# Kernel optimization log

Measured on AMD Instinct MI355X. Metric: run time of the kernel, lower is better.

The kernel has to match this reference:

```python
import jax, jax.numpy as jnp
import numpy as np

# --- static config ---
B = 64        # graphs per batch
NPG = 512     # nodes per graph
N = B * NPG   # total nodes = 32768
EPG = 8192    # edges per graph (avg degree 16)
E = B * EPG   # total edges = 524288
L = 16        # tokens per node
V = 50000     # vocab
H = 256       # hidden_size == rnn hidden_size
P = 128       # projection_dim
K1 = 256      # ceil(0.5 * 512) nodes kept after pool 1
K2 = 128      # ceil(0.5 * 256) nodes kept after pool 2
PAD = 0


def setup_inputs() -> dict:
    key = jax.random.key(0)
    ks = jax.random.split(key, 16)
    tokens = jax.random.randint(ks[0], (N, L), 0, V, dtype=jnp.int32)
    eg = jnp.repeat(jnp.arange(B, dtype=jnp.int32), EPG)  # graph id per edge
    src = jax.random.randint(ks[1], (E,), 0, NPG, dtype=jnp.int32) + eg * NPG
    dst = jax.random.randint(ks[2], (E,), 0, NPG, dtype=jnp.int32) + eg * NPG
    edge_attr = jax.random.uniform(ks[3], (E, 2), dtype=jnp.float32)
    sH = 1.0 / np.sqrt(H).astype(np.float32)
    sP = 1.0 / np.sqrt(P).astype(np.float32)
    return {
        'tokens': tokens, 'src': src, 'dst': dst, 'edge_attr': edge_attr,
        'emb': jax.random.normal(ks[4], (V, H), jnp.float32) * 0.05,
        'W0': jax.random.normal(ks[5], (H, H), jnp.float32) * sH,
        'b0': jnp.zeros((H,), jnp.float32),
        'W1': jax.random.normal(ks[6], (H, H), jnp.float32) * sH,
        'b1': jnp.zeros((H,), jnp.float32),
        'p0': jax.random.normal(ks[7], (H,), jnp.float32),
        'p1': jax.random.normal(ks[8], (H,), jnp.float32),
        'wg': jax.random.normal(ks[9], (H, 1), jnp.float32) * sH,
        'bg': jnp.zeros((1,), jnp.float32),
        'Wp1': jax.random.normal(ks[10], (H, P), jnp.float32) * sH,
        'bp1': jnp.zeros((P,), jnp.float32),
        'Wp2': jax.random.normal(ks[11], (P, P), jnp.float32) * sP,
        'bp2': jnp.zeros((P,), jnp.float32),
    }


def _st_encode(tokens, emb):
    # STEncoder proxy: embed token ids, masked mean over non-pad tokens -> [N, H]
    mask = (tokens != PAD).astype(jnp.float32)  # [N, L]
    e = emb[tokens] * mask[..., None]           # [N, L, H]
    cnt = jnp.maximum(mask.sum(-1, keepdims=True), 1.0)
    return e.sum(1) / cnt


def _gcn(x, W, b, src, dst, w, n):
    # GCNConv with edge weights + self loops (fill 1), symmetric normalization
    h = x @ W                                        # [n, H]
    deg = jax.ops.segment_sum(w, dst, num_segments=n) + 1.0
    dinv = jax.lax.rsqrt(deg)
    norm = dinv[src] * w * dinv[dst]                 # [E]
    agg = jax.ops.segment_sum(h[src] * norm[:, None], dst, num_segments=n)
    return agg + h * (1.0 / deg)[:, None] + b


def _topk_pool(x, p, src, dst, w, n_per, k):
    # TopKPooling: score = x.p/||p||, keep top-k per graph, gate by tanh(score)
    G = x.shape[0] // n_per
    score = (x @ p) / jnp.linalg.norm(p)
    vals, idx = jax.lax.top_k(score.reshape(G, n_per), k)   # [G, k]
    perm = (idx + (jnp.arange(G, dtype=jnp.int32) * n_per)[:, None]).reshape(-1)
    x_new = x[perm] * jnp.tanh(vals.reshape(-1))[:, None]
    new_of_old = jnp.full((G * n_per,), -1, jnp.int32).at[perm].set(
        jnp.arange(G * k, dtype=jnp.int32))
    ns, nd = new_of_old[src], new_of_old[dst]
    keep = (ns >= 0) & (nd >= 0)
    # masked edges: weight 0 -> contribute nothing (== subgraph filtering)
    return (x_new, jnp.where(keep, ns, 0), jnp.where(keep, nd, 0),
            jnp.where(keep, w, 0.0))


def _attpool(x, wg, bg, k):
    # GlobalAttention: softmax(Linear(x,1)) over each graph's nodes
    G = x.shape[0] // k
    gate = (x @ wg + bg).reshape(G, k)        # [G, k]
    a = jax.nn.softmax(gate, axis=1)
    return jnp.einsum('gk,gkh->gh', a, x.reshape(G, k, x.shape[-1]))


def reference(tokens, src, dst, edge_attr, emb, W0, b0, W1, b1, p0, p1,
              wg, bg, Wp1, bp1, Wp2, bp2):
    w = edge_attr.mean(axis=1)                 # GCN path: scalar edge weights
    x = _st_encode(tokens, emb)                # [N, H]
    # layer 1
    x = jax.nn.relu(_gcn(x, W0, b0, src, dst, w, N))
    x, src1, dst1, w1 = _topk_pool(x, p0, src, dst, w, NPG, K1)
    out = _attpool(x, wg, bg, K1)              # [B, H]
    # hidden layer
    x = jax.nn.relu(_gcn(x, W1, b1, src1, dst1, w1, B * K1))
    x, _, _, _ = _topk_pool(x, p1, src1, dst1, w1, K1, K2)
    out = out + _attpool(x, wg, bg, K2)
    # projection head + L2 normalize
    h = jax.nn.relu(out @ Wp1 + bp1)
    logits = h @ Wp2 + bp2
    logits = logits / jnp.maximum(
        jnp.linalg.norm(logits, axis=-1, keepdims=True), 1e-12)
    return (logits, out)
```

## Files before the change

kernel.cpp:

```cpp
#include <hip/hip_runtime.h>
#include <hip/hip_bf16.h>

constexpr int C_B   = 64;
constexpr int C_NPG = 512;
constexpr int C_N   = 32768;
constexpr int C_E   = 524288;
constexpr int C_L   = 16;
constexpr int C_H   = 256;
constexpr int C_P   = 128;
constexpr int C_K1  = 256;
constexpr int C_K2  = 128;
constexpr int C_V   = 50000;

typedef __attribute__((ext_vector_type(8)))  short  short8;
typedef __attribute__((ext_vector_type(16))) float  float16;
typedef unsigned short ushort;
typedef unsigned int   uint;

__device__ inline void split_bf16(float x, ushort& h, ushort& l) {
    __hip_bfloat16 bh = __float2bfloat16(x);
    float fh = __bfloat162float(bh);
    __hip_bfloat16 bl = __float2bfloat16(x - fh);
    h = __builtin_bit_cast(ushort, bh);
    l = __builtin_bit_cast(ushort, bl);
}

__device__ inline ushort f2h(float x) {
    return __builtin_bit_cast(ushort, (_Float16)x);
}
__device__ inline float4 h4_to_f4(ushort4 v) {
    return make_float4((float)__builtin_bit_cast(_Float16, v.x),
                       (float)__builtin_bit_cast(_Float16, v.y),
                       (float)__builtin_bit_cast(_Float16, v.z),
                       (float)__builtin_bit_cast(_Float16, v.w));
}

__global__ void k_pre(const float* __restrict__ emb, ushort* __restrict__ emb16,
                      const float* __restrict__ ea, const int* __restrict__ dst,
                      float* __restrict__ w, float* __restrict__ degb, int* __restrict__ indegb,
                      const float* __restrict__ W0, const float* __restrict__ W1,
                      ushort* __restrict__ W0h, ushort* __restrict__ W0l,
                      ushort* __restrict__ W1h, ushort* __restrict__ W1l,
                      const float* __restrict__ p0, const float* __restrict__ p1,
                      float* __restrict__ invnp) {
    int b = blockIdx.x, t = threadIdx.x;
    __shared__ float r[256];
    if (b < 6250) {
        int i = (b * 256 + t) * 8;
        float4 a = *(const float4*)&emb[i];
        float4 c = *(const float4*)&emb[i + 4];
        short8 o;
        o[0] = (short)f2h(a.x); o[1] = (short)f2h(a.y);
        o[2] = (short)f2h(a.z); o[3] = (short)f2h(a.w);
        o[4] = (short)f2h(c.x); o[5] = (short)f2h(c.y);
        o[6] = (short)f2h(c.z); o[7] = (short)f2h(c.w);
        *(short8*)&emb16[i] = o;
    } else if (b < 8298) {
        int e = (b - 6250) * 256 + t;
        float ww = 0.5f * (ea[2 * e] + ea[2 * e + 1]);
        w[e] = ww;
        int d = dst[e];
        atomicAdd(&degb[d], ww);
        atomicAdd(&indegb[d], 1);
    } else if (b < 8810) {
        int g = (b - 8298) * 256 + t;
        int which = g >> 16;
        int idx = g & 65535;
        int k = idx >> 8, n = idx & 255;
        float x = (which ? W1 : W0)[idx];
        ushort h, l;
        split_bf16(x, h, l);
        size_t a = ((size_t)(n >> 5) * 16 + (k >> 4)) * 512 + ((k >> 3) & 1) * 256
                 + (n & 31) * 8 + (k & 7);
        if (which) { W1h[a] = h; W1l[a] = l; }
        else       { W0h[a] = h; W0l[a] = l; }
    } else {
        const float* p = (b == 8810) ? p0 : p1;
        float v = p[t];
        r[t] = v * v; __syncthreads();
        for (int s = 128; s; s >>= 1) { if (t < s) r[t] += r[t + s]; __syncthreads(); }
        if (t == 0) invnp[b - 8810] = rsqrtf(r[0]);
    }
}

template <int NPER>
__global__ void k_scan(const int* __restrict__ indeg, int* __restrict__ rowstart,
                       int* __restrict__ cursor, float* __restrict__ deg,
                       float* __restrict__ dinv) {
    int g = blockIdx.x, t = threadIdx.x;
    int node = g * NPER + t;
    float d = deg[node] + 1.f;
    dinv[node] = rsqrtf(d);
    deg[node]  = 1.f / d;
    __shared__ int s[NPER];
    int v = indeg[node];
    s[t] = v;
    __syncthreads();
    for (int off = 1; off < NPER; off <<= 1) {
        int add = (t >= off) ? s[t - off] : 0;
        __syncthreads();
        s[t] += add;
        __syncthreads();
    }
    int start = g * 8192 + s[t] - v;
    rowstart[node] = start;
    cursor[node]   = start;
}

__global__ void k_csr_scatter(const int* __restrict__ src, const int* __restrict__ dst,
                              const float* __restrict__ w, const float* __restrict__ dinv,
                              int* __restrict__ cursor, int* __restrict__ csr_src,
                              float* __restrict__ csr_nrm) {
    int e = blockIdx.x * blockDim.x + threadIdx.x;
    if (e >= C_E) return;
    int s = src[e], d = dst[e];
    int slot = atomicAdd(&cursor[d], 1);
    csr_src[slot] = s;
    csr_nrm[slot] = dinv[s] * w[e] * dinv[d];
}

__global__ __launch_bounds__(256)
void k_gcn_gather(const ushort* __restrict__ Hm, const int* __restrict__ rowstart,
                  const int* __restrict__ indeg, const int* __restrict__ csr_src,
                  const float* __restrict__ csr_nrm, const float* __restrict__ selfw,
                  const float* __restrict__ bias, const float* __restrict__ p,
                  const float* __restrict__ invnp, float* __restrict__ Xout,
                  float* __restrict__ score, int nnodes) {
    int n    = (blockIdx.x * blockDim.x + threadIdx.x) >> 6;
    int lane = threadIdx.x & 63;
    if (n >= nnodes) return;
    int h4 = lane * 4;
    float4 hv = h4_to_f4(*(const ushort4*)&Hm[(size_t)n * C_H + h4]);
    float  sw = selfw[n];
    float4 bv = *(const float4*)&bias[h4];
    float4 acc = make_float4(fmaf(hv.x, sw, bv.x), fmaf(hv.y, sw, bv.y),
                             fmaf(hv.z, sw, bv.z), fmaf(hv.w, sw, bv.w));
    int start = rowstart[n], cnt = indeg[n];
    const int*   sp = csr_src + start;
    const float* np = csr_nrm + start;
    #pragma unroll 4
    for (int j = 0; j < cnt; ++j) {
        int   s  = sp[j];
        float nm = np[j];
        float4 xv = h4_to_f4(*(const ushort4*)&Hm[(size_t)s * C_H + h4]);
        acc.x = fmaf(nm, xv.x, acc.x);
        acc.y = fmaf(nm, xv.y, acc.y);
        acc.z = fmaf(nm, xv.z, acc.z);
        acc.w = fmaf(nm, xv.w, acc.w);
    }
    acc.x = fmaxf(acc.x, 0.f); acc.y = fmaxf(acc.y, 0.f);
    acc.z = fmaxf(acc.z, 0.f); acc.w = fmaxf(acc.w, 0.f);
    *(float4*)&Xout[(size_t)n * C_H + h4] = acc;
    float4 pv = *(const float4*)&p[h4];
    float s = acc.x * pv.x + acc.y * pv.y + acc.z * pv.z + acc.w * pv.w;
    #pragma unroll
    for (int m = 32; m; m >>= 1) s += __shfl_xor(s, m, 64);
    if (lane == 0) score[n] = s * invnp[0];
}

__global__ __launch_bounds__(256)
void k_st_encode4(const int* __restrict__ tokens, const ushort* __restrict__ emb16,
                  ushort* __restrict__ Xh, ushort* __restrict__ Xl) {
    __shared__ float Xs[32 * 257];
    __shared__ int tokS[512];
    int tid = threadIdx.x;
    int blk = blockIdx.x;
    tokS[tid]       = tokens[(size_t)blk * 512 + tid];
    tokS[tid + 256] = tokens[(size_t)blk * 512 + tid + 256];
    __syncthreads();
    int w    = tid >> 6;
    int lane = tid & 63;
    for (int i = 0; i < 8; ++i) {
        int nl = w * 8 + i;
        float4 acc = make_float4(0.f, 0.f, 0.f, 0.f);
        int cnt = 0;
        #pragma unroll
        for (int t = 0; t < C_L; ++t) {
            int tk = tokS[nl * 16 + t];
            if (tk != 0) {
                float4 ev = h4_to_f4(*(const ushort4*)&emb16[(size_t)tk * C_H + lane * 4]);
                acc.x += ev.x; acc.y += ev.y; acc.z += ev.z; acc.w += ev.w;
                cnt++;
            }
        }
        float inv = 1.f / fmaxf((float)cnt, 1.f);
        float* xr = &Xs[nl * 257 + lane * 4];
        xr[0] = acc.x * inv; xr[1] = acc.y * inv;
        xr[2] = acc.z * inv; xr[3] = acc.w * inv;
    }
    __syncthreads();
    #pragma unroll
    for (int i = 0; i < 4; ++i) {
        int c    = tid + 256 * i;
        int kst  = c >> 6;
        int ln   = c & 63;
        int ml   = ln & 31;
        int kb   = kst * 16 + (ln >> 5) * 8;
        short8 hv, lv;
        #pragma unroll
        for (int j = 0; j < 8; ++j) {
            ushort h, l;
            split_bf16(Xs[ml * 257 + kb + j], h, l);
            hv[j] = (short)h; lv[j] = (short)l;
        }
        size_t base = (size_t)blk * 8192 + (size_t)c * 8;
        *(short8*)&Xh[base] = hv;
        *(short8*)&Xl[base] = lv;
    }
}

__global__ __launch_bounds__(256)
void k_gemm_mfma(const ushort* __restrict__ Ah, const ushort* __restrict__ Al,
                 const ushort* __restrict__ Bh, const ushort* __restrict__ Bl,
                 ushort* __restrict__ C) {
    __shared__ short lds[16384];
    int tid  = threadIdx.x;
    int lane = tid & 63;
    int wid  = tid >> 6;
    int wm   = wid & 1, wn = wid >> 1;
    int mb   = blockIdx.x;
    int nb   = blockIdx.y;

    float16 acc[2][2];
    #pragma unroll
    for (int mi = 0; mi < 2; ++mi)
        #pragma unroll
        for (int ni = 0; ni < 2; ++ni)
            #pragma unroll
            for (int r = 0; r < 16; ++r) acc[mi][ni][r] = 0.f;

    for (int kc = 0; kc < 8; ++kc) {
        __syncthreads();
        #pragma unroll
        for (int i = 0; i < 4; ++i) {
            int a  = tid + 256 * i;
            int s  = a >> 9;
            int mt = (a >> 7) & 3;
            int k2 = (a >> 6) & 1;
            int ln = a & 63;
            const ushort* ap = (s ? Al : Ah)
                + (((size_t)(mb * 4 + mt) * 16 + kc * 2 + k2) * 64 + ln) * 8;
            *(int4*)&lds[a * 8] = *(const int4*)ap;
            const ushort* bp = (s ? Bl : Bh)
                + (((size_t)(nb * 4 + mt) * 16 + kc * 2 + k2) * 64 + ln) * 8;
            *(int4*)&lds[8192 + a * 8] = *(const int4*)bp;
        }
        __syncthreads();
        #pragma unroll
        for (int k2 = 0; k2 < 2; ++k2) {
            short8 ah[2], al[2], bh[2], bl[2];
            #pragma unroll
            for (int mi = 0; mi < 2; ++mi) {
                int mt = wm * 2 + mi;
                ah[mi] = *(short8*)&lds[((mt * 2 + k2) * 64 + lane) * 8];
                al[mi] = *(short8*)&lds[(((4 + mt) * 2 + k2) * 64 + lane) * 8];
            }
            #pragma unroll
            for (int ni = 0; ni < 2; ++ni) {
                int nt = wn * 2 + ni;
                bh[ni] = *(short8*)&lds[8192 + ((nt * 2 + k2) * 64 + lane) * 8];
                bl[ni] = *(short8*)&lds[8192 + (((4 + nt) * 2 + k2) * 64 + lane) * 8];
            }
            #pragma unroll
            for (int mi = 0; mi < 2; ++mi)
                #pragma unroll
                for (int ni = 0; ni < 2; ++ni) {
                    acc[mi][ni] = __builtin_amdgcn_mfma_f32_32x32x16_bf16(
                        ah[mi], bh[ni], acc[mi][ni], 0, 0, 0);
                    acc[mi][ni] = __builtin_amdgcn_mfma_f32_32x32x16_bf16(
                        ah[mi], bl[ni], acc[mi][ni], 0, 0, 0);
                    acc[mi][ni] = __builtin_amdgcn_mfma_f32_32x32x16_bf16(
                        al[mi], bh[ni], acc[mi][ni], 0, 0, 0);
                }
        }
    }
    int col = lane & 31;
    int rquad = 4 * (lane >> 5);
    #pragma unroll
    for (int mi = 0; mi < 2; ++mi)
        #pragma unroll
        for (int ni = 0; ni < 2; ++ni) {
            int mbase = mb * 128 + wm * 64 + mi * 32;
            int nbase = nb * 128 + wn * 64 + ni * 32 + col;
            #pragma unroll
            for (int r = 0; r < 16; ++r) {
                int row = (r & 3) + 8 * (r >> 2) + rquad;
                C[(size_t)(mbase + row) * C_H + nbase] = f2h(acc[mi][ni][r]);
            }
        }
}

__global__ __launch_bounds__(512)
void k_pool1_fused(const float* __restrict__ score, const float* __restrict__ X,
                   const int* __restrict__ src, const int* __restrict__ dst,
                   const float* __restrict__ wbuf,
                   const float* __restrict__ wg, const float* __restrict__ bg,
                   ushort* __restrict__ XFh, ushort* __restrict__ XFl,
                   float* __restrict__ outb,
                   float* __restrict__ selfw1, int* __restrict__ rowst1,
                   int* __restrict__ indeg1, int* __restrict__ csrs,
                   float* __restrict__ csrn) {
    int g = blockIdx.x, t = threadIdx.x;
    __shared__ float sv[C_NPG];
    __shared__ int   si[C_NPG];
    __shared__ int   nooL[C_NPG];
    __shared__ int   olds[C_K1];
    __shared__ float gt[C_K1];
    __shared__ float sd[C_K1];
    __shared__ float red[C_K1];
    __shared__ float an[C_K1];
    __shared__ float Xs[32 * 257];
    __shared__ int   indegL[C_K1];
    __shared__ float degL[C_K1];
    __shared__ float dinvL[C_K1];
    __shared__ int   rowstL[C_K1];
    __shared__ int   cursL[C_K1];

    sv[t] = score[g * C_NPG + t];
    si[t] = t;
    __syncthreads();
    for (int k = 2; k <= C_NPG; k <<= 1)
        for (int j = k >> 1; j > 0; j >>= 1) {
            int ixj = t ^ j;
            if (ixj > t) {
                bool desc = ((t & k) == 0);
                float a = sv[t], b = sv[ixj];
                if (desc ? (a < b) : (a > b)) {
                    sv[t] = b; sv[ixj] = a;
                    int tmp = si[t]; si[t] = si[ixj]; si[ixj] = tmp;
                }
            }
            __syncthreads();
        }
    nooL[si[t]] = (t < C_K1) ? t : -1;
    if (t < C_K1) {
        olds[t]   = si[t];
        gt[t]     = tanhf(sv[t]);
        indegL[t] = 0;
        degL[t]   = 0.f;
    }
    __syncthreads();

    int w = t >> 6, lane = t & 63;
    float4 wg4 = *(const float4*)&wg[lane * 4];
    float bgv = bg[0];
    for (int r = w; r < C_K1; r += 8) {
        float4 xv = *(const float4*)&X[(size_t)(g * C_NPG + olds[r]) * C_H + lane * 4];
        float s = xv.x * wg4.x + xv.y * wg4.y + xv.z * wg4.z + xv.w * wg4.w;
        #pragma unroll
        for (int m = 32; m; m >>= 1) s += __shfl_xor(s, m, 64);
        if (lane == 0) sd[r] = gt[r] * s + bgv;
    }
    __syncthreads();
    if (t < C_K1) red[t] = sd[t];
    __syncthreads();
    for (int s = 128; s; s >>= 1) { if (t < s) red[t] = fmaxf(red[t], red[t + s]); __syncthreads(); }
    float mx = red[0];
    __syncthreads();
    if (t < C_K1) { float ex = expf(sd[t] - mx); an[t] = ex; red[t] = ex; }
    __syncthreads();
    for (int s = 128; s; s >>= 1) { if (t < s) red[t] += red[t + s]; __syncthreads(); }
    if (t < C_K1) an[t] = an[t] / red[0] * gt[t];
    __syncthreads();
    {
        int h = t & 255, half = t >> 8;
        float acc = 0.f;
        for (int n = half * 128; n < half * 128 + 128; ++n)
            acc = fmaf(an[n], X[(size_t)(g * C_NPG + olds[n]) * C_H + h], acc);
        __syncthreads();
        if (half == 1) sd[h] = acc;
        __syncthreads();
        if (half == 0) outb[g * C_H + h] = acc + sd[h];
    }
    __syncthreads();

    for (int c = 0; c < 8; ++c) {
        #pragma unroll
        for (int i = 0; i < 4; ++i) {
            int u  = t + 512 * i;
            int nl = u >> 6, ln = u & 63;
            int r  = c * 32 + nl;
            float4 v = *(const float4*)&X[(size_t)(g * C_NPG + olds[r]) * C_H + ln * 4];
            float gg = gt[r];
            float* xr = &Xs[nl * 257 + ln * 4];
            xr[0] = v.x * gg; xr[1] = v.y * gg; xr[2] = v.z * gg; xr[3] = v.w * gg;
        }
        __syncthreads();
        #pragma unroll
        for (int i = 0; i < 2; ++i) {
            int cch = t + 512 * i;
            int kst = cch >> 6, ln = cch & 63;
            int ml  = ln & 31;
            int kb  = kst * 16 + (ln >> 5) * 8;
            short8 hv, lv;
            #pragma unroll
            for (int j = 0; j < 8; ++j) {
                ushort h, l;
                split_bf16(Xs[ml * 257 + kb + j], h, l);
                hv[j] = (short)h; lv[j] = (short)l;
            }
            size_t base = (size_t)(g * 8 + c) * 8192 + (size_t)cch * 8;
            *(short8*)&XFh[base] = hv;
            *(short8*)&XFl[base] = lv;
        }
        __syncthreads();
    }

    for (int i = 0; i < 16; ++i) {
        int e  = g * 8192 + t + 512 * i;
        int ns = nooL[src[e] - g * C_NPG];
        int nd = nooL[dst[e] - g * C_NPG];
        if (ns >= 0 && nd >= 0) {
            atomicAdd(&indegL[nd], 1);
            unsafeAtomicAdd(&degL[nd], wbuf[e]);
        }
    }
    __syncthreads();
    if (t < C_K1) {
        float d = degL[t] + 1.f;
        dinvL[t] = rsqrtf(d);
        selfw1[g * C_K1 + t] = 1.f / d;
        indeg1[g * C_K1 + t] = indegL[t];
        rowstL[t] = indegL[t];
    }
    __syncthreads();
    for (int off = 1; off < C_K1; off <<= 1) {
        int add = 0;
        if (t < C_K1 && t >= off) add = rowstL[t - off];
        __syncthreads();
        if (t < C_K1) rowstL[t] += add;
        __syncthreads();
    }
    if (t < C_K1) {
        int start = g * 8192 + rowstL[t] - indegL[t];
        rowstL[t] = start;
        cursL[t]  = start;
        rowst1[g * C_K1 + t] = start;
    }
    __syncthreads();
    for (int i = 0; i < 16; ++i) {
        int e  = g * 8192 + t + 512 * i;
        int ns = nooL[src[e] - g * C_NPG];
        int nd = nooL[dst[e] - g * C_NPG];
        if (ns >= 0 && nd >= 0) {
            int slot = atomicAdd(&cursL[nd], 1);
            csrs[slot] = g * C_K1 + ns;
            csrn[slot] = dinvL[ns] * wbuf[e] * dinvL[nd];
        }
    }
}

__global__ __launch_bounds__(256)
void k_pool2_fused(const float* __restrict__ score, const float* __restrict__ X,
                   const float* __restrict__ wg, const float* __restrict__ bg,
                   float* __restrict__ outb) {
    int g = blockIdx.x, t = threadIdx.x;
    __shared__ float sv[C_K1];
    __shared__ int   si[C_K1];
    __shared__ int   olds[C_K2];
    __shared__ float gt[C_K2];
    __shared__ float sd[C_K2];
    __shared__ float red[C_K2];
    __shared__ float an[C_K2];
    sv[t] = score[g * C_K1 + t];
    si[t] = t;
    __syncthreads();
    for (int k = 2; k <= C_K1; k <<= 1)
        for (int j = k >> 1; j > 0; j >>= 1) {
            int ixj = t ^ j;
            if (ixj > t) {
                bool desc = ((t & k) == 0);
                float a = sv[t], b = sv[ixj];
                if (desc ? (a < b) : (a > b)) {
                    sv[t] = b; sv[ixj] = a;
                    int tmp = si[t]; si[t] = si[ixj]; si[ixj] = tmp;
                }
            }
            __syncthreads();
        }
    if (t < C_K2) { olds[t] = si[t]; gt[t] = tanhf(sv[t]); }
    __syncthreads();
    int w = t >> 6, lane = t & 63;
    float4 wg4 = *(const float4*)&wg[lane * 4];
    float bgv = bg[0];
    for (int r = w; r < C_K2; r += 4) {
        float4 xv = *(const float4*)&X[(size_t)(g * C_K1 + olds[r]) * C_H + lane * 4];
        float s = xv.x * wg4.x + xv.y * wg4.y + xv.z * wg4.z + xv.w * wg4.w;
        #pragma unroll
        for (int m = 32; m; m >>= 1) s += __shfl_xor(s, m, 64);
        if (lane == 0) sd[r] = gt[r] * s + bgv;
    }
    __syncthreads();
    if (t < C_K2) red[t] = sd[t];
    __syncthreads();
    for (int s = 64; s; s >>= 1) { if (t < s) red[t] = fmaxf(red[t], red[t + s]); __syncthreads(); }
    float mx = red[0];
    __syncthreads();
    if (t < C_K2) { float ex = expf(sd[t] - mx); an[t] = ex; red[t] = ex; }
    __syncthreads();
    for (int s = 64; s; s >>= 1) { if (t < s) red[t] += red[t + s]; __syncthreads(); }
    if (t < C_K2) an[t] = an[t] / red[0] * gt[t];
    __syncthreads();
    float acc = 0.f;
    for (int n = 0; n < C_K2; ++n)
        acc = fmaf(an[n], X[(size_t)(g * C_K1 + olds[n]) * C_H + t], acc);
    outb[g * C_H + t] += acc;
}

__global__ void k_head(const float* __restrict__ outb, const float* __restrict__ Wp1,
                       const float* __restrict__ bp1, const float* __restrict__ Wp2,
                       const float* __restrict__ bp2, float* __restrict__ dout) {
    int g = blockIdx.x;
    int t = threadIdx.x;
    __shared__ float so[C_H];
    so[t] = outb[g * C_H + t];
    so[t + 128] = outb[g * C_H + t + 128];
    __syncthreads();
    float acc = bp1[t];
    for (int k = 0; k < C_H; ++k) acc += so[k] * Wp1[k * C_P + t];
    float hv = fmaxf(acc, 0.f);
    __shared__ float sh[C_P];
    sh[t] = hv; __syncthreads();
    float lg = bp2[t];
    for (int k = 0; k < C_P; ++k) lg += sh[k] * Wp2[k * C_P + t];
    __shared__ float red[C_P];
    red[t] = lg * lg; __syncthreads();
    for (int s = 64; s > 0; s >>= 1) { if (t < s) red[t] += red[t + s]; __syncthreads(); }
    float nrm = fmaxf(sqrtf(red[0]), 1e-12f);
    dout[g * C_P + t] = lg / nrm;
    dout[C_B * C_P + g * C_H + t]       = so[t];
    dout[C_B * C_P + g * C_H + t + 128] = so[t + 128];
}

extern "C" void kernel_launch(void* const* d_in, const int* in_sizes, int n_in,
                              void* d_out, int out_size, void* d_ws, size_t ws_size,
                              hipStream_t stream) {
    const int*   tokens = (const int*)d_in[0];
    const int*   src    = (const int*)d_in[1];
    const int*   dst    = (const int*)d_in[2];
    const float* eattr  = (const float*)d_in[3];
    const float* emb    = (const float*)d_in[4];
    const float* W0     = (const float*)d_in[5];
    const float* b0     = (const float*)d_in[6];
    const float* W1     = (const float*)d_in[7];
    const float* b1     = (const float*)d_in[8];
    const float* p0     = (const float*)d_in[9];
    const float* p1     = (const float*)d_in[10];
    const float* wg     = (const float*)d_in[11];
    const float* bg     = (const float*)d_in[12];
    const float* Wp1    = (const float*)d_in[13];
    const float* bp1    = (const float*)d_in[14];
    const float* Wp2    = (const float*)d_in[15];
    const float* bp2    = (const float*)d_in[16];
    float* out = (float*)d_out;

    float* f = (float*)d_ws;
    size_t o = 0;
    float*  XB    = f + o; o += (size_t)C_N * C_H;
    float*  HB    = f + o; o += (size_t)C_N * C_H;
    ushort* XFh   = (ushort*)(f + o); o += (size_t)C_N * C_H / 2;
    ushort* XFl   = (ushort*)(f + o); o += (size_t)C_N * C_H / 2;
    float*  wbuf  = f + o; o += C_E;
    float*  degb  = f + o; o += C_N;
    int*    indegb= (int*)(f + o); o += C_N;
    float*  dinv  = f + o; o += C_N;
    int*    rowst = (int*)(f + o); o += C_N;
    int*    curs  = (int*)(f + o); o += C_N;
    int*    csrs  = (int*)(f + o); o += C_E;
    float*  csrn  = f + o; o += C_E;
    float*  deg1  = f + o; o += C_B * C_K1;
    int*    indeg1= (int*)(f + o); o += C_B * C_K1;
    int*    rowst1= (int*)(f + o); o += C_B * C_K1;
    float*  outb  = f + o; o += C_B * C_H;
    float*  score = f + o; o += C_N;
    float*  invnp = f + o; o += 16;
    ushort* W0h   = (ushort*)(f + o); o += C_H * C_H / 2;
    ushort* W0l   = (ushort*)(f + o); o += C_H * C_H / 2;
    ushort* W1h   = (ushort*)(f + o); o += C_H * C_H / 2;
    ushort* W1l   = (ushort*)(f + o); o += C_H * C_H / 2;

    ushort* emb16 = (ushort*)XB;
    float*  AGG1  = XB;
    ushort* Hhf   = (ushort*)HB;

    hipMemsetAsync(degb, 0, 2 * C_N * sizeof(float), stream);

    k_pre<<<8812, 256, 0, stream>>>(emb, emb16, eattr, dst, wbuf, degb, indegb,
                                    W0, W1, W0h, W0l, W1h, W1l, p0, p1, invnp);
    k_st_encode4<<<C_N / 32, 256, 0, stream>>>(tokens, emb16, XFh, XFl);
    k_scan<C_NPG><<<C_B, C_NPG, 0, stream>>>(indegb, rowst, curs, degb, dinv);
    k_csr_scatter<<<C_E / 256, 256, 0, stream>>>(src, dst, wbuf, dinv, curs, csrs, csrn);

    k_gemm_mfma<<<dim3(C_N / 128, 2), 256, 0, stream>>>(XFh, XFl, W0h, W0l, Hhf);
    k_gcn_gather<<<(C_N * 64) / 256, 256, 0, stream>>>(
        Hhf, rowst, indegb, csrs, csrn, degb, b0, p0, invnp, XB, score, C_N);

    k_pool1_fused<<<C_B, 512, 0, stream>>>(
        score, XB, src, dst, wbuf, wg, bg, XFh, XFl, outb,
        deg1, rowst1, indeg1, csrs, csrn);

    k_gemm_mfma<<<dim3((C_B * C_K1) / 128, 2), 256, 0, stream>>>(XFh, XFl, W1h, W1l, Hhf);
    k_gcn_gather<<<(C_B * C_K1 * 64) / 256, 256, 0, stream>>>(
        Hhf, rowst1, indeg1, csrs, csrn, deg1, b1, p1, invnp + 1, AGG1, score, C_B * C_K1);

    k_pool2_fused<<<C_B, C_K1, 0, stream>>>(score, AGG1, wg, bg, outb);

    k_head<<<C_B, C_P, 0, stream>>>(outb, Wp1, bp1, Wp2, bp2, out);
}
```

Before: 405.7 us.

## Cut barriers in pool kernels with register bitonic sort and wave reductions

The two top-k pooling kernels now sort in registers, using wave shuffles for strides under 64 and shared memory only for larger strides. Tree reductions for the softmax max and sum become single-wave shuffle reductions. The gate dot product and the attention-weighted sum are restructured to use float4 loads with a per-wave partial-sum buffer. The shared-memory staging for the bf16 split is replaced by direct gathers. Edge data from the first pass is kept in registers for the CSR fill, and the prefix scan uses wave shuffles. Together these remove many __syncthreads and repeated global loads, at the cost of higher register pressure in a 512-thread block.

```diff
diff --git a/kernel.cpp b/kernel.cpp
--- a/kernel.cpp
+++ b/kernel.cpp
@@ -33,6 +33,31 @@
                        (float)__builtin_bit_cast(_Float16, v.y),
                        (float)__builtin_bit_cast(_Float16, v.z),
                        (float)__builtin_bit_cast(_Float16, v.w));
+}
+
+template <int NPER>
+__device__ inline void bitonic_desc(float& v, int& idx, float* svL, int* siL, int t) {
+    #pragma unroll
+    for (int k = 2; k <= NPER; k <<= 1) {
+        bool desc = ((t & k) == 0);
+        #pragma unroll
+        for (int j = k >> 1; j > 0; j >>= 1) {
+            bool amLo = ((t & j) == 0);
+            bool keepMax = (desc == amLo);
+            float pv; int pi;
+            if (j >= 64) {
+                __syncthreads();
+                svL[t] = v; siL[t] = idx;
+                __syncthreads();
+                pv = svL[t ^ j]; pi = siL[t ^ j];
+            } else {
+                pv = __shfl_xor(v, j, 64);
+                pi = __shfl_xor(idx, j, 64);
+            }
+            bool take = keepMax ? (pv > v) : (pv < v);
+            if (take) { v = pv; idx = pi; }
+        }
+    }
 }
 
 __global__ void k_pre(const float* __restrict__ emb, ushort* __restrict__ emb16,
@@ -301,118 +326,127 @@
                    int* __restrict__ indeg1, int* __restrict__ csrs,
                    float* __restrict__ csrn) {
     int g = blockIdx.x, t = threadIdx.x;
-    __shared__ float sv[C_NPG];
-    __shared__ int   si[C_NPG];
+    int lane = t & 63, w = t >> 6;
+    __shared__ float svL[C_NPG];
+    __shared__ int   siL[C_NPG];
     __shared__ int   nooL[C_NPG];
     __shared__ int   olds[C_K1];
     __shared__ float gt[C_K1];
     __shared__ float sd[C_K1];
     __shared__ float red[C_K1];
     __shared__ float an[C_K1];
-    __shared__ float Xs[32 * 257];
+    __shared__ float wsum[8][C_H];
     __shared__ int   indegL[C_K1];
     __shared__ float degL[C_K1];
     __shared__ float dinvL[C_K1];
-    __shared__ int   rowstL[C_K1];
     __shared__ int   cursL[C_K1];
 
-    sv[t] = score[g * C_NPG + t];
-    si[t] = t;
-    __syncthreads();
-    for (int k = 2; k <= C_NPG; k <<= 1)
-        for (int j = k >> 1; j > 0; j >>= 1) {
-            int ixj = t ^ j;
-            if (ixj > t) {
-                bool desc = ((t & k) == 0);
-                float a = sv[t], b = sv[ixj];
-                if (desc ? (a < b) : (a > b)) {
-                    sv[t] = b; sv[ixj] = a;
-                    int tmp = si[t]; si[t] = si[ixj]; si[ixj] = tmp;
-                }
-            }
-            __syncthreads();
-        }
-    nooL[si[t]] = (t < C_K1) ? t : -1;
+    float v = score[g * C_NPG + t];
+    int   idx = t;
+    bitonic_desc<C_NPG>(v, idx, svL, siL, t);
+    __syncthreads();
+    nooL[idx] = (t < C_K1) ? t : -1;
     if (t < C_K1) {
-        olds[t]   = si[t];
-        gt[t]     = tanhf(sv[t]);
+        olds[t]   = idx;
+        gt[t]     = tanhf(v);
         indegL[t] = 0;
         degL[t]   = 0.f;
     }
     __syncthreads();
 
-    int w = t >> 6, lane = t & 63;
-    float4 wg4 = *(const float4*)&wg[lane * 4];
     float bgv = bg[0];
-    for (int r = w; r < C_K1; r += 8) {
-        float4 xv = *(const float4*)&X[(size_t)(g * C_NPG + olds[r]) * C_H + lane * 4];
-        float s = xv.x * wg4.x + xv.y * wg4.y + xv.z * wg4.z + xv.w * wg4.w;
-        #pragma unroll
-        for (int m = 32; m; m >>= 1) s += __shfl_xor(s, m, 64);
-        if (lane == 0) sd[r] = gt[r] * s + bgv;
-    }
-    __syncthreads();
-    if (t < C_K1) red[t] = sd[t];
-    __syncthreads();
-    for (int s = 128; s; s >>= 1) { if (t < s) red[t] = fmaxf(red[t], red[t + s]); __syncthreads(); }
+    {
+        int r = t >> 1, half = t & 1;
+        const float* xr = &X[(size_t)(g * C_NPG + olds[r]) * C_H + half * 128];
+        const float* wr = &wg[half * 128];
+        float s = 0.f;
+        #pragma unroll
+        for (int kk = 0; kk < 128; kk += 4) {
+            float4 xv = *(const float4*)&xr[kk];
+            float4 wv = *(const float4*)&wr[kk];
+            s += xv.x * wv.x + xv.y * wv.y + xv.z * wv.z + xv.w * wv.w;
+        }
+        if (half) red[r] = s;
+        __syncthreads();
+        if (!half) sd[r] = gt[r] * (s + red[r]) + bgv;
+        __syncthreads();
+    }
+    if (w == 0) {
+        float m = fmaxf(fmaxf(sd[lane], sd[lane + 64]), fmaxf(sd[lane + 128], sd[lane + 192]));
+        #pragma unroll
+        for (int mm = 32; mm; mm >>= 1) m = fmaxf(m, __shfl_xor(m, mm, 64));
+        if (lane == 0) red[0] = m;
+    }
+    __syncthreads();
     float mx = red[0];
-    __syncthreads();
-    if (t < C_K1) { float ex = expf(sd[t] - mx); an[t] = ex; red[t] = ex; }
-    __syncthreads();
-    for (int s = 128; s; s >>= 1) { if (t < s) red[t] += red[t + s]; __syncthreads(); }
-    if (t < C_K1) an[t] = an[t] / red[0] * gt[t];
+    if (t < C_K1) an[t] = expf(sd[t] - mx);
+    __syncthreads();
+    if (w == 0) {
+        float s4 = an[lane] + an[lane + 64] + an[lane + 128] + an[lane + 192];
+        #pragma unroll
+        for (int mm = 32; mm; mm >>= 1) s4 += __shfl_xor(s4, mm, 64);
+        if (lane == 0) red[1] = s4;
+    }
+    __syncthreads();
+    if (t < C_K1) an[t] = an[t] / red[1] * gt[t];
     __syncthreads();
     {
-        int h = t & 255, half = t >> 8;
-        float acc = 0.f;
-        for (int n = half * 128; n < half * 128 + 128; ++n)
-            acc = fmaf(an[n], X[(size_t)(g * C_NPG + olds[n]) * C_H + h], acc);
-        __syncthreads();
-        if (half == 1) sd[h] = acc;
-        __syncthreads();
-        if (half == 0) outb[g * C_H + h] = acc + sd[h];
-    }
-    __syncthreads();
-
-    for (int c = 0; c < 8; ++c) {
-        #pragma unroll
-        for (int i = 0; i < 4; ++i) {
-            int u  = t + 512 * i;
-            int nl = u >> 6, ln = u & 63;
-            int r  = c * 32 + nl;
-            float4 v = *(const float4*)&X[(size_t)(g * C_NPG + olds[r]) * C_H + ln * 4];
-            float gg = gt[r];
-            float* xr = &Xs[nl * 257 + ln * 4];
-            xr[0] = v.x * gg; xr[1] = v.y * gg; xr[2] = v.z * gg; xr[3] = v.w * gg;
-        }
-        __syncthreads();
-        #pragma unroll
-        for (int i = 0; i < 2; ++i) {
-            int cch = t + 512 * i;
-            int kst = cch >> 6, ln = cch & 63;
-            int ml  = ln & 31;
-            int kb  = kst * 16 + (ln >> 5) * 8;
-            short8 hv, lv;
-            #pragma unroll
-            for (int j = 0; j < 8; ++j) {
-                ushort h, l;
-                split_bf16(Xs[ml * 257 + kb + j], h, l);
-                hv[j] = (short)h; lv[j] = (short)l;
-            }
-            size_t base = (size_t)(g * 8 + c) * 8192 + (size_t)cch * 8;
-            *(short8*)&XFh[base] = hv;
-            *(short8*)&XFl[base] = lv;
-        }
-        __syncthreads();
-    }
-
+        float4 a4 = make_float4(0.f, 0.f, 0.f, 0.f);
+        #pragma unroll 4
+        for (int r = 0; r < 32; ++r) {
+            int rr = w * 32 + r;
+            float a = an[rr];
+            float4 xv = *(const float4*)&X[(size_t)(g * C_NPG + olds[rr]) * C_H + lane * 4];
+            a4.x = fmaf(a, xv.x, a4.x); a4.y = fmaf(a, xv.y, a4.y);
+            a4.z = fmaf(a, xv.z, a4.z); a4.w = fmaf(a, xv.w, a4.w);
+        }
+        *(float4*)&wsum[w][lane * 4] = a4;
+        __syncthreads();
+        if (t < C_H) {
+            float s = wsum[0][t] + wsum[1][t] + wsum[2][t] + wsum[3][t]
+                    + wsum[4][t] + wsum[5][t] + wsum[6][t] + wsum[7][t];
+            outb[g * C_H + t] = s;
+        }
+    }
+
+    #pragma unroll
+    for (int i = 0; i < 16; ++i) {
+        int u   = t + 512 * i;
+        int mt  = u >> 10;
+        int c   = u & 1023;
+        int kst = c >> 6, ln = c & 63, ml = ln & 31;
+        int kb  = kst * 16 + (ln >> 5) * 8;
+        int r   = mt * 32 + ml;
+        const float* xp = &X[(size_t)(g * C_NPG + olds[r]) * C_H + kb];
+        float gg = gt[r];
+        float4 a = *(const float4*)&xp[0];
+        float4 b = *(const float4*)&xp[4];
+        float e8[8] = {a.x * gg, a.y * gg, a.z * gg, a.w * gg,
+                       b.x * gg, b.y * gg, b.z * gg, b.w * gg};
+        short8 hv, lv;
+        #pragma unroll
+        for (int j = 0; j < 8; ++j) {
+            ushort h, l;
+            split_bf16(e8[j], h, l);
+            hv[j] = (short)h; lv[j] = (short)l;
+        }
+        size_t base = (size_t)(g * 8 + mt) * 8192 + (size_t)c * 8;
+        *(short8*)&XFh[base] = hv;
+        *(short8*)&XFl[base] = lv;
+    }
+
+    int   nsR[16], ndR[16];
+    float wwR[16];
+    #pragma unroll
     for (int i = 0; i < 16; ++i) {
         int e  = g * 8192 + t + 512 * i;
         int ns = nooL[src[e] - g * C_NPG];
         int nd = nooL[dst[e] - g * C_NPG];
+        float ww = wbuf[e];
+        nsR[i] = ns; ndR[i] = nd; wwR[i] = ww;
         if (ns >= 0 && nd >= 0) {
             atomicAdd(&indegL[nd], 1);
-            unsafeAtomicAdd(&degL[nd], wbuf[e]);
+            unsafeAtomicAdd(&degL[nd], ww);
         }
     }
     __syncthreads();
@@ -421,31 +455,35 @@
         dinvL[t] = rsqrtf(d);
         selfw1[g * C_K1 + t] = 1.f / d;
         indeg1[g * C_K1 + t] = indegL[t];
-        rowstL[t] = indegL[t];
-    }
-    __syncthreads();
-    for (int off = 1; off < C_K1; off <<= 1) {
-        int add = 0;
-        if (t < C_K1 && t >= off) add = rowstL[t - off];
-        __syncthreads();
-        if (t < C_K1) rowstL[t] += add;
-        __syncthreads();
-    }
-    if (t < C_K1) {
-        int start = g * 8192 + rowstL[t] - indegL[t];
-        rowstL[t] = start;
-        cursL[t]  = start;
-        rowst1[g * C_K1 + t] = start;
-    }
-    __syncthreads();
+    }
+    if (w == 0) {
+        int a0 = indegL[lane * 4], a1 = indegL[lane * 4 + 1];
+        int a2 = indegL[lane * 4 + 2], a3 = indegL[lane * 4 + 3];
+        int s4 = a0 + a1 + a2 + a3;
+        int sc = s4;
+        #pragma unroll
+        for (int off = 1; off < 64; off <<= 1) {
+            int pv = __shfl_up(sc, off, 64);
+            if (lane >= off) sc += pv;
+        }
+        int base = g * 8192 + (sc - s4);
+        cursL[lane * 4]     = base;
+        cursL[lane * 4 + 1] = base + a0;
+        cursL[lane * 4 + 2] = base + a0 + a1;
+        cursL[lane * 4 + 3] = base + a0 + a1 + a2;
+        rowst1[g * C_K1 + lane * 4]     = base;
+        rowst1[g * C_K1 + lane * 4 + 1] = base + a0;
+        rowst1[g * C_K1 + lane * 4 + 2] = base + a0 + a1;
+        rowst1[g * C_K1 + lane * 4 + 3] = base + a0 + a1 + a2;
+    }
+    __syncthreads();
+    #pragma unroll
     for (int i = 0; i < 16; ++i) {
-        int e  = g * 8192 + t + 512 * i;
-        int ns = nooL[src[e] - g * C_NPG];
-        int nd = nooL[dst[e] - g * C_NPG];
+        int ns = nsR[i], nd = ndR[i];
         if (ns >= 0 && nd >= 0) {
             int slot = atomicAdd(&cursL[nd], 1);
             csrs[slot] = g * C_K1 + ns;
-            csrn[slot] = dinvL[ns] * wbuf[e] * dinvL[nd];
+            csrn[slot] = dinvL[ns] * wwR[i] * dinvL[nd];
         }
     }
 }
@@ -455,56 +493,74 @@
                    const float* __restrict__ wg, const float* __restrict__ bg,
                    float* __restrict__ outb) {
     int g = blockIdx.x, t = threadIdx.x;
-    __shared__ float sv[C_K1];
-    __shared__ int   si[C_K1];
+    int lane = t & 63, w = t >> 6;
+    __shared__ float svL[C_K1];
+    __shared__ int   siL[C_K1];
     __shared__ int   olds[C_K2];
     __shared__ float gt[C_K2];
     __shared__ float sd[C_K2];
     __shared__ float red[C_K2];
     __shared__ float an[C_K2];
-    sv[t] = score[g * C_K1 + t];
-    si[t] = t;
-    __syncthreads();
-    for (int k = 2; k <= C_K1; k <<= 1)
-        for (int j = k >> 1; j > 0; j >>= 1) {
-            int ixj = t ^ j;
-            if (ixj > t) {
-                bool desc = ((t & k) == 0);
-                float a = sv[t], b = sv[ixj];
-                if (desc ? (a < b) : (a > b)) {
-                    sv[t] = b; sv[ixj] = a;
-                    int tmp = si[t]; si[t] = si[ixj]; si[ixj] = tmp;
-                }
-            }
-            __syncthreads();
-        }
-    if (t < C_K2) { olds[t] = si[t]; gt[t] = tanhf(sv[t]); }
-    __syncthreads();
-    int w = t >> 6, lane = t & 63;
-    float4 wg4 = *(const float4*)&wg[lane * 4];
+    __shared__ float wsum[4][C_H];
+
+    float v = score[g * C_K1 + t];
+    int   idx = t;
+    bitonic_desc<C_K1>(v, idx, svL, siL, t);
+    __syncthreads();
+    if (t < C_K2) { olds[t] = idx; gt[t] = tanhf(v); }
+    __syncthreads();
+
     float bgv = bg[0];
-    for (int r = w; r < C_K2; r += 4) {
-        float4 xv = *(const float4*)&X[(size_t)(g * C_K1 + olds[r]) * C_H + lane * 4];
-        float s = xv.x * wg4.x + xv.y * wg4.y + xv.z * wg4.z + xv.w * wg4.w;
-        #pragma unroll
-        for (int m = 32; m; m >>= 1) s += __shfl_xor(s, m, 64);
-        if (lane == 0) sd[r] = gt[r] * s + bgv;
-    }
-    __syncthreads();
-    if (t < C_K2) red[t] = sd[t];
-    __syncthreads();
-    for (int s = 64; s; s >>= 1) { if (t < s) red[t] = fmaxf(red[t], red[t + s]); __syncthreads(); }
+    {
+        int r = t >> 1, half = t & 1;
+        const float* xr = &X[(size_t)(g * C_K1 + olds[r]) * C_H + half * 128];
+        const float* wr = &wg[half * 128];
+        float s = 0.f;
+        #pragma unroll
+        for (int kk = 0; kk < 128; kk += 4) {
+            float4 xv = *(const float4*)&xr[kk];
+            float4 wv = *(const float4*)&wr[kk];
+            s += xv.x * wv.x + xv.y * wv.y + xv.z * wv.z + xv.w * wv.w;
+        }
+        if (half) red[r] = s;
+        __syncthreads();
+        if (!half) sd[r] = gt[r] * (s + red[r]) + bgv;
+        __syncthreads();
+    }
+    if (w == 0) {
+        float m = fmaxf(sd[lane], sd[lane + 64]);
+        #pragma unroll
+        for (int mm = 32; mm; mm >>= 1) m = fmaxf(m, __shfl_xor(m, mm, 64));
+        if (lane == 0) red[0] = m;
+    }
+    __syncthreads();
     float mx = red[0];
-    __syncthreads();
-    if (t < C_K2) { float ex = expf(sd[t] - mx); an[t] = ex; red[t] = ex; }
-    __syncthreads();
-    for (int s = 64; s; s >>= 1) { if (t < s) red[t] += red[t + s]; __syncthreads(); }
-    if (t < C_K2) an[t] = an[t] / red[0] * gt[t];
-    __syncthreads();
-    float acc = 0.f;
-    for (int n = 0; n < C_K2; ++n)
-        acc = fmaf(an[n], X[(size_t)(g * C_K1 + olds[n]) * C_H + t], acc);
-    outb[g * C_H + t] += acc;
+    if (t < C_K2) an[t] = expf(sd[t] - mx);
+    __syncthreads();
+    if (w == 0) {
+        float s2 = an[lane] + an[lane + 64];
+        #pragma unroll
+        for (int mm = 32; mm; mm >>= 1) s2 += __shfl_xor(s2, mm, 64);
+        if (lane == 0) red[1] = s2;
+    }
+    __syncthreads();
+    if (t < C_K2) an[t] = an[t] / red[1] * gt[t];
+    __syncthreads();
+    {
+        float4 a4 = make_float4(0.f, 0.f, 0.f, 0.f);
+        #pragma unroll 4
+        for (int r = 0; r < 32; ++r) {
+            int rr = w * 32 + r;
+            float a = an[rr];
+            float4 xv = *(const float4*)&X[(size_t)(g * C_K1 + olds[rr]) * C_H + lane * 4];
+            a4.x = fmaf(a, xv.x, a4.x); a4.y = fmaf(a, xv.y, a4.y);
+            a4.z = fmaf(a, xv.z, a4.z); a4.w = fmaf(a, xv.w, a4.w);
+        }
+        *(float4*)&wsum[w][lane * 4] = a4;
+        __syncthreads();
+        float s = wsum[0][t] + wsum[1][t] + wsum[2][t] + wsum[3][t];
+        outb[g * C_H + t] += s;
+    }
 }
 
 __global__ void k_head(const float* __restrict__ outb, const float* __restrict__ Wp1,
```

Measured after the change: 375.3 us. 1.08x faster.
